# Kernel optimization log

Hardware: AMD Instinct MI355X
Metric: run time of the kernel (lower is better)

Reference implementation:

```python
import jax, jax.numpy as jnp
import numpy as np

B, S, D, F, E, CAP = 4, 2048, 1024, 4096, 8, 320


def setup_inputs() -> dict:
    key = jax.random.key(0)
    k1, k2, k3, k4 = jax.random.split(key, 4)
    return {
        "hidden_states": jax.random.normal(k1, (B, S, D), dtype=jnp.float32),
        "router_w": jax.random.normal(k2, (D, E), dtype=jnp.float32) * 0.02,
        "wi": jax.random.normal(k3, (E, D, F), dtype=jnp.float32) * 0.02,
        "wo": jax.random.normal(k4, (E, F, D), dtype=jnp.float32) * 0.02,
    }


def reference(hidden_states, router_w, wi, wo):
    # ---- Router (Switch top-1 with per-sequence expert capacity) ----
    b, s, d = hidden_states.shape
    e = router_w.shape[1]
    logits = hidden_states.astype(jnp.float32) @ router_w          # [B,S,E]
    probs = jax.nn.softmax(logits, axis=-1)                        # [B,S,E]
    expert_idx = jnp.argmax(probs, axis=-1)                        # [B,S]
    onehot = jax.nn.one_hot(expert_idx, e, dtype=jnp.int32)        # [B,S,E]
    priority = jnp.cumsum(onehot, axis=1)                          # cumsum over seq dim (dim=-2)
    keep = onehot * (priority <= CAP).astype(jnp.int32)            # capacity-masked router_mask

    # slot of each token within its chosen expert (0-based)
    slot = jnp.take_along_axis(priority, expert_idx[..., None], axis=-1)[..., 0] - 1  # [B,S]
    valid = slot < CAP                                             # dropped tokens exceed capacity
    slot_sc = jnp.where(valid, slot, CAP)                          # out-of-range -> dropped by scatter

    b_ar = jnp.broadcast_to(jnp.arange(b)[:, None], (b, s))
    s_ar = jnp.broadcast_to(jnp.arange(s)[None, :], (b, s))
    dispatch = jnp.zeros((b, e, CAP), jnp.int32).at[b_ar, expert_idx, slot_sc].set(
        s_ar.astype(jnp.int32), mode="drop")                       # [B,E,CAP] token index per slot
    slot_used = jnp.zeros((b, e, CAP), bool).at[b_ar, expert_idx, slot_sc].set(
        valid, mode="drop")                                        # [B,E,CAP]

    # ---- Dispatch: gather tokens into [B,E,CAP,D] ----
    xg = jax.vmap(lambda xb, ib: xb[ib])(hidden_states, dispatch)  # [B,E,CAP,D]

    # ---- Per-expert dense FFN (grouped GEMM) ----
    hg = jax.nn.relu(jnp.einsum("becd,edf->becf", xg, wi))         # [B,E,CAP,F]
    yg = jnp.einsum("becf,efd->becd", hg, wo)                      # [B,E,CAP,D]

    # ---- Combine: scatter expert outputs back; unrouted tokens keep input ----
    idx_back = jnp.where(slot_used, dispatch, s)                   # out-of-range -> dropped
    next_states = jax.vmap(
        lambda xb, ib, yb: xb.at[ib.reshape(-1)].set(yb.reshape(-1, d), mode="drop")
    )(hidden_states, idx_back, yg)                                 # [B,S,D]

    max_prob = jnp.max(probs, axis=-1, keepdims=True)              # [B,S,1]
    out = max_prob * next_states
    expert_index_out = jnp.argmax(keep, axis=-1)                   # [B,S] (0 for dropped tokens)
    return out, logits, expert_index_out
```

## Files before the change

### kernel.cpp

```cpp
#include <hip/hip_runtime.h>
#include <hip/hip_bf16.h>
#include <stdint.h>

#define B_ 4
#define S_ 2048
#define D_ 1024
#define F_ 4096
#define E_ 8
#define CAP_ 320
#define BS_ (B_*S_)
#define MPE 1280

typedef unsigned short u16;
typedef __attribute__((ext_vector_type(8))) short bf16x8;
typedef __attribute__((ext_vector_type(4))) float f32x4;
typedef __attribute__((ext_vector_type(4))) unsigned short u16x4;
typedef __attribute__((ext_vector_type(8))) unsigned short u16x8;

__device__ __forceinline__ u16 f2bf(float f) {
  union { float f; uint32_t u; } v; v.f = f;
  uint32_t r = (v.u + 0x7FFFu + ((v.u >> 16) & 1u)) >> 16;
  return (u16)r;
}

__device__ __forceinline__ void gload16(const void* g, void* l) {
  __builtin_amdgcn_global_load_lds(
      (const __attribute__((address_space(1))) uint32_t*)g,
      (__attribute__((address_space(3))) uint32_t*)l, 16, 0, 0);
}

__device__ __forceinline__ void transpose_block(
    const float* __restrict__ W, u16* __restrict__ WT,
    const int K, const int N, const int bid, void* ldsraw)
{
  float (*tile)[65] = (float(*)[65])ldsraw;
  const int tk = K >> 7, tn = N >> 6;
  const int e = bid / (tk * tn), r = bid % (tk * tn);
  const int k0 = (r / tn) << 7, n0 = (r % tn) << 6;
  const float* We = W + (size_t)e * K * N;
  u16* WTe = WT + (size_t)e * N * K;
  const int t = threadIdx.x;
  const int fr = t >> 2, c0 = (t & 3) * 16;
#pragma unroll
  for (int j = 0; j < 4; ++j) {
    const float4 v = *(const float4*)(We + (size_t)(k0 + fr) * N + n0 + c0 + j * 4);
    tile[fr][c0 + j*4 + 0] = v.x; tile[fr][c0 + j*4 + 1] = v.y;
    tile[fr][c0 + j*4 + 2] = v.z; tile[fr][c0 + j*4 + 3] = v.w;
  }
  __syncthreads();
  const int nr = t >> 3, kk0 = (t & 7) * 16;
  u16x8 o0, o1;
#pragma unroll
  for (int j = 0; j < 8; ++j) o0[j] = f2bf(tile[kk0 + j][nr]);
#pragma unroll
  for (int j = 0; j < 8; ++j) o1[j] = f2bf(tile[kk0 + 8 + j][nr]);
  u16* dst = WTe + (size_t)(n0 + nr) * K + k0 + kk0;
  *(u16x8*)dst = o0;
  *(u16x8*)(dst + 8) = o1;
}

__global__ __launch_bounds__(512) void transpose_kernel(
    const float* __restrict__ W, u16* __restrict__ WT, const int K, const int N)
{
  __shared__ __align__(16) float tile[128][65];
  transpose_block(W, WT, K, N, blockIdx.x, (void*)tile);
}

__global__ __launch_bounds__(512) void prep_kernel(
    const float* __restrict__ hs, const float* __restrict__ rw,
    const float* __restrict__ wi, u16* __restrict__ wT,
    float* __restrict__ logits, float* __restrict__ maxp,
    int* __restrict__ eidx, const int twiT)
{
  __shared__ __align__(16) float tile[128][65];
  if ((int)blockIdx.x < twiT) {
    transpose_block(wi, wT, D_, F_, blockIdx.x, (void*)tile);
    return;
  }
  const int wv = threadIdx.x >> 6, l = threadIdx.x & 63;
  const int token = (blockIdx.x - twiT) * 8 + wv;
  const float* row = hs + (size_t)token * D_;
  const float4* rw4 = (const float4*)rw;

  double acc0=0, acc1=0, acc2=0, acc3=0, acc4=0, acc5=0, acc6=0, acc7=0;
#pragma unroll
  for (int j = 0; j < 4; ++j) {
    const int d4 = l + j * 64;
    const float4 v = ((const float4*)row)[d4];
#pragma unroll
    for (int c = 0; c < 4; ++c) {
      const int d = d4 * 4 + c;
      const float x = (&v.x)[c];
      const float4 w0 = rw4[d * 2];
      const float4 w1 = rw4[d * 2 + 1];
      acc0 += (double)x * (double)w0.x;
      acc1 += (double)x * (double)w0.y;
      acc2 += (double)x * (double)w0.z;
      acc3 += (double)x * (double)w0.w;
      acc4 += (double)x * (double)w1.x;
      acc5 += (double)x * (double)w1.y;
      acc6 += (double)x * (double)w1.z;
      acc7 += (double)x * (double)w1.w;
    }
  }
  double acc[E_] = {acc0, acc1, acc2, acc3, acc4, acc5, acc6, acc7};
#pragma unroll
  for (int e = 0; e < E_; ++e) {
#pragma unroll
    for (int off = 32; off; off >>= 1)
      acc[e] += __shfl_xor(acc[e], off);
  }
  if (l == 0) {
    float lg[E_];
#pragma unroll
    for (int e = 0; e < E_; ++e) lg[e] = (float)acc[e];
    float lmax = lg[0]; int am = 0;
#pragma unroll
    for (int e = 1; e < E_; ++e) { if (lg[e] > lmax) { lmax = lg[e]; am = e; } }
    float sum = 0.f;
#pragma unroll
    for (int e = 0; e < E_; ++e) sum += expf(lg[e] - lmax);
#pragma unroll
    for (int e = 0; e < E_; ++e) logits[(size_t)token * E_ + e] = lg[e];
    maxp[token] = 1.0f / sum;
    eidx[token] = am;
  }
}

__global__ __launch_bounds__(256) void scan_kernel(
    const int* __restrict__ eidx, int* __restrict__ tok,
    float* __restrict__ eout, const float* __restrict__ hs,
    const float* __restrict__ maxp, float* __restrict__ out)
{
  const int b = blockIdx.x >> 3, e = blockIdx.x & 7;
  __shared__ int wsum[4];
  const int tid = threadIdx.x, wv = tid >> 6, l = tid & 63;
  for (int i = tid; i < CAP_; i += 256) tok[(b * E_ + e) * CAP_ + i] = -1;
  __syncthreads();
  int base = 0;
  for (int ch = 0; ch < S_ / 256; ++ch) {
    const int s = ch * 256 + tid;
    const bool p = (eidx[b * S_ + s] == e);
    const unsigned long long m = __ballot(p);
    const int lp = __popcll(m & ((1ULL << l) - 1ULL));
    if (l == 0) wsum[wv] = __popcll(m);
    __syncthreads();
    int pre = 0, tot = 0;
#pragma unroll
    for (int w = 0; w < 4; ++w) { if (w < wv) pre += wsum[w]; tot += wsum[w]; }
    if (p) {
      const int rank = base + pre + lp;
      if (rank < CAP_) {
        tok[(b * E_ + e) * CAP_ + rank] = s;
        eout[b * S_ + s] = (float)e;
      } else {
        eout[b * S_ + s] = 0.0f;
        const float mp = maxp[b * S_ + s];
        const float4* src = (const float4*)(hs + (size_t)(b * S_ + s) * D_);
        float4* dst = (float4*)(out + (size_t)(b * S_ + s) * D_);
        for (int j = 0; j < D_ / 4; ++j) {
          const float4 vv = src[j];
          float4 o; o.x = vv.x * mp; o.y = vv.y * mp; o.z = vv.z * mp; o.w = vv.w * mp;
          dst[j] = o;
        }
      }
    }
    base += tot;
    __syncthreads();
  }
}

__global__ __launch_bounds__(256) void gather_kernel(
    const float* __restrict__ hs, const int* __restrict__ tok,
    u16* __restrict__ Xg)
{
  const int bx = blockIdx.x;
  const int e = bx / MPE, r = bx % MPE;
  const int b = r / CAP_, c = r % CAP_;
  const int t = tok[(b * E_ + e) * CAP_ + c];
  const int d = threadIdx.x * 4;
  u16x4 o;
  if (t >= 0) {
    const float4 vv = *(const float4*)(hs + ((size_t)(b * S_ + t)) * D_ + d);
    o[0] = f2bf(vv.x); o[1] = f2bf(vv.y); o[2] = f2bf(vv.z); o[3] = f2bf(vv.w);
  } else {
    o[0] = 0; o[1] = 0; o[2] = 0; o[3] = 0;
  }
  *(u16x4*)(Xg + (size_t)bx * D_ + d) = o;
}

template<int MODE>
__global__ __launch_bounds__(512, 2) void moe_gemm8(
    const u16* __restrict__ Aall, const u16* __restrict__ Btall,
    u16* __restrict__ hgout, float* __restrict__ out,
    const int* __restrict__ tok, const float* __restrict__ maxp,
    const int K, const int ntn, const int gemm_blocks,
    const float* __restrict__ Wtr, u16* __restrict__ WTtr,
    const int tK, const int tN)
{
  __shared__ __align__(16) u16 lds[2][2][2][8192];

  if ((int)blockIdx.x >= gemm_blocks) {
    transpose_block(Wtr, WTtr, tK, tN, blockIdx.x - gemm_blocks, (void*)lds);
    return;
  }

  const int cpx = gemm_blocks >> 3;
  const int bid = blockIdx.x;
  const int swzb = (bid & 7) * cpx + (bid >> 3);
  const int bpe = 5 * ntn;
  const int e = swzb / bpe, rem = swzb % bpe;
  const int m0 = (rem / ntn) * 256, n0 = (rem % ntn) * 256;
  const int N = ntn * 256;

  const u16* Ae = Aall + (size_t)e * MPE * K;
  const u16* Be = Btall + (size_t)e * N * K;

  const int tid = threadIdx.x;
  const int wv = tid >> 6, l = tid & 63;
  const int wr = wv >> 2, wc = wv & 3;
  const int lr = l & 15, lk = l >> 4;
  const int rswz = ((lr >> 3) & 1) << 4;
  const int gs0 = tid ^ (((tid >> 5) & 1) << 1);
  const size_t goff = (size_t)((gs0 >> 2) & 127) * K + (size_t)((gs0 & 3) * 8);
  const int dwoff = wv * 512;

  const u16* pA0 = Ae + (size_t)m0 * K;
  const u16* pA1 = Ae + (size_t)(m0 + 128) * K;
  const u16* pB0 = Be + (size_t)n0 * K;
  const u16* pB1 = Be + (size_t)(n0 + 128) * K;

  const int NT = K >> 6;

  f32x4 acc[8][4];
#pragma unroll
  for (int i = 0; i < 8; ++i)
#pragma unroll
    for (int j = 0; j < 4; ++j) acc[i][j] = (f32x4){0.f, 0.f, 0.f, 0.f};

  bf16x8 fa[8], fb0[4], fb1[4];

#define LDSH(p, ab, h) (&lds[p][ab][h][0])

#define STAGE(dhalf, rb, tt) do {                                          \
    const u16* s_ = (rb) + goff + (size_t)((tt) * 64);                     \
    gload16(s_,      (dhalf) + dwoff);                                     \
    gload16(s_ + 32, (dhalf) + 4096 + dwoff);                              \
  } while (0)

#define READ_A(msub, p) do {                                               \
    _Pragma("unroll")                                                      \
    for (int mf = 0; mf < 4; ++mf)                                         \
      _Pragma("unroll")                                                    \
      for (int kk = 0; kk < 2; ++kk)                                       \
        fa[mf*2+kk] = *(const bf16x8*)&lds[p][0][wr]                       \
            [(kk*128 + (msub)*64 + mf*16 + lr)*32 + ((lk*8) ^ rswz)];      \
  } while (0)

#define READ_B(nsub, p, fb) do {                                           \
    _Pragma("unroll")                                                      \
    for (int nf = 0; nf < 2; ++nf)                                         \
      _Pragma("unroll")                                                    \
      for (int kk = 0; kk < 2; ++kk)                                       \
        fb[nf*2+kk] = *(const bf16x8*)&lds[p][1][wc>>1]                    \
            [(kk*128 + (wc&1)*64 + (nsub)*32 + nf*16 + lr)*32              \
             + ((lk*8) ^ rswz)];                                           \
  } while (0)

#define MFMA_Q(msub, nsub, fb) do {                                        \
    __builtin_amdgcn_s_setprio(1);                                         \
    _Pragma("unroll")                                                      \
    for (int mf = 0; mf < 4; ++mf)                                         \
      _Pragma("unroll")                                                    \
      for (int nf = 0; nf < 2; ++nf)                                       \
        _Pragma("unroll")                                                  \
        for (int kk = 0; kk < 2; ++kk)                                     \
          acc[(msub)*4+mf][(nsub)*2+nf] =                                  \
              __builtin_amdgcn_mfma_f32_16x16x32_bf16(                     \
                  fa[mf*2+kk], fb[nf*2+kk],                                \
                  acc[(msub)*4+mf][(nsub)*2+nf], 0, 0, 0);                 \
    __builtin_amdgcn_s_setprio(0);                                         \
  } while (0)

#define BAR() __builtin_amdgcn_s_barrier()
#define LGKM0() do { asm volatile("s_waitcnt lgkmcnt(0)" ::: "memory");    \
                     __builtin_amdgcn_sched_barrier(0); } while (0)
#define LGKM4() do { asm volatile("s_waitcnt lgkmcnt(4)" ::: "memory");    \
                     __builtin_amdgcn_sched_barrier(0); } while (0)
#define VM6() asm volatile("s_waitcnt vmcnt(6)" ::: "memory")
#define VM0() asm volatile("s_waitcnt vmcnt(0)" ::: "memory")

#define DO_TILE(p, pn, tc) do {                                            \
                                                                  \
    READ_A(0, p); READ_B(0, p, fb0); READ_B(1, p, fb1);                    \
    if ((tc) + 1 < NT) STAGE(LDSH(pn, 0, 1), pA1, (tc) + 1);               \
    BAR();                                                                 \
    LGKM4();                                                               \
    MFMA_Q(0, 0, fb0);                                                     \
    LGKM0();                                                               \
    MFMA_Q(0, 1, fb1);                                                     \
    BAR();                                                                 \
                                                                  \
    READ_A(1, p);                                                          \
    if ((tc) + 2 < NT) {                                                   \
      STAGE(LDSH(p, 1, 0), pB0, (tc) + 2);                                 \
      STAGE(LDSH(p, 1, 1), pB1, (tc) + 2);                                 \
      STAGE(LDSH(p, 0, 0), pA0, (tc) + 2);                                 \
    }                                                                      \
    BAR();                                                                 \
    LGKM0();                                                               \
    MFMA_Q(1, 0, fb0);                                                     \
    MFMA_Q(1, 1, fb1);                                                     \
    if ((tc) >= NT - 2) VM0(); else VM6();                                 \
    BAR();                                                                 \
  } while (0)

  STAGE(LDSH(0, 0, 0), pA0, 0);
  STAGE(LDSH(0, 0, 1), pA1, 0);
  STAGE(LDSH(0, 1, 0), pB0, 0);
  STAGE(LDSH(0, 1, 1), pB1, 0);
  STAGE(LDSH(1, 1, 0), pB0, 1);
  STAGE(LDSH(1, 1, 1), pB1, 1);
  STAGE(LDSH(1, 0, 0), pA0, 1);
  VM6(); BAR();

  for (int t = 0; t < NT; t += 2) {
    DO_TILE(0, 1, t);
    DO_TILE(1, 0, t + 1);
  }

  if (MODE == 1) {
#pragma unroll
    for (int i = 0; i < 8; ++i) {
#pragma unroll
      for (int r = 0; r < 4; ++r) {
        const int grow = m0 + wr * 128 + i * 16 + lk * 4 + r;
        u16* hrow = hgout + ((size_t)e * MPE + grow) * (size_t)N + n0 + wc * 64;
#pragma unroll
        for (int j = 0; j < 4; ++j)
          hrow[j * 16 + lr] = f2bf(fmaxf(acc[i][j][r], 0.0f));
      }
    }
  } else {
#pragma unroll
    for (int i = 0; i < 8; ++i) {
#pragma unroll
      for (int r = 0; r < 4; ++r) {
        const int grow = m0 + wr * 128 + i * 16 + lk * 4 + r;
        const int b = grow / CAP_, c = grow % CAP_;
        const int t = tok[(b * E_ + e) * CAP_ + c];
        if (t >= 0) {
          const float sc = maxp[b * S_ + t];
          float* orow = out + ((size_t)(b * S_ + t)) * D_ + n0 + wc * 64;
#pragma unroll
          for (int j = 0; j < 4; ++j)
            orow[j * 16 + lr] = sc * acc[i][j][r];
        }
      }
    }
  }
#undef LDSH
#undef STAGE
#undef READ_A
#undef READ_B
#undef MFMA_Q
#undef BAR
#undef LGKM0
#undef LGKM4
#undef VM6
#undef VM0
#undef DO_TILE
}

extern "C" void kernel_launch(void* const* d_in, const int* in_sizes, int n_in,
                              void* d_out, int out_size, void* d_ws, size_t ws_size,
                              hipStream_t stream)
{
  const float* hs = (const float*)d_in[0];
  const float* rw = (const float*)d_in[1];
  const float* wi = (const float*)d_in[2];
  const float* wo = (const float*)d_in[3];

  float* out    = (float*)d_out;
  float* logits = out + (size_t)BS_ * D_;
  float* eout   = logits + (size_t)BS_ * E_;

  uint8_t* ws = (uint8_t*)d_ws;
  int*   tok  = (int*)(ws + 0);
  float* maxp = (float*)(ws + 40960);
  int*   eidx = (int*)(ws + 73728);
  u16*   Xg   = (u16*)(ws + 131072);
  u16*   hg   = (u16*)(ws + 21102592);
  u16*   wiT  = (u16*)(ws + 104988672);
  if (ws_size < 172097536ULL) return;
  const bool big = ws_size >= 239206400ULL;
  u16* woT = big ? (u16*)(ws + 172097536) : wiT;

  const int twiT = E_ * (D_ / 128) * (F_ / 64);
  const int twoT = E_ * (F_ / 128) * (D_ / 64);
  const int g1 = E_ * 5 * (F_ / 256);
  const int g2 = E_ * 5 * (D_ / 256);

  prep_kernel<<<twiT + BS_ / 8, 512, 0, stream>>>(
      hs, rw, wi, wiT, logits, maxp, eidx, twiT);
  scan_kernel<<<B_ * E_, 256, 0, stream>>>(eidx, tok, eout, hs, maxp, out);
  gather_kernel<<<E_ * MPE, 256, 0, stream>>>(hs, tok, Xg);

  if (big) {
    moe_gemm8<1><<<g1 + twoT, 512, 0, stream>>>(
        Xg, wiT, hg, nullptr, tok, maxp, D_, F_ / 256, g1, wo, woT, F_, D_);
  } else {
    moe_gemm8<1><<<g1, 512, 0, stream>>>(
        Xg, wiT, hg, nullptr, tok, maxp, D_, F_ / 256, g1,
        nullptr, nullptr, 0, 0);
    transpose_kernel<<<twoT, 512, 0, stream>>>(wo, woT, F_, D_);
  }
  moe_gemm8<2><<<g2, 512, 0, stream>>>(
      hg, woT, nullptr, out, tok, maxp, F_, D_ / 256, g2,
      nullptr, nullptr, 0, 0);
}
```

Measured before the change: 354.7 us.

## Shrink GEMM tiles to 128x128 with 256-thread blocks and new pipeline

Replaces the 256x256-tile, 512-thread grouped GEMM with a 128x128-tile, 4-wave kernel. It uses a new interleaved LDS read / MFMA / prefetch schedule with quarter-wise A fragment loads and double-buffered staging. The transpose and prep kernels also move to 256-thread blocks, with each thread handling twice the elements. The aim is more blocks for better CU fill on the small expert GEMMs (1280 rows per expert), at the cost of lower per-block data reuse and more global traffic.

```diff
diff --git a/kernel.cpp b/kernel.cpp
--- a/kernel.cpp
+++ b/kernel.cpp
@@ -29,7 +29,7 @@
       (__attribute__((address_space(3))) uint32_t*)l, 16, 0, 0);
 }
 
-__device__ __forceinline__ void transpose_block(
+__device__ __forceinline__ void transpose_block256(
     const float* __restrict__ W, u16* __restrict__ WT,
     const int K, const int N, const int bid, void* ldsraw)
 {
@@ -40,33 +40,33 @@
   const float* We = W + (size_t)e * K * N;
   u16* WTe = WT + (size_t)e * N * K;
   const int t = threadIdx.x;
-  const int fr = t >> 2, c0 = (t & 3) * 16;
-#pragma unroll
-  for (int j = 0; j < 4; ++j) {
+  const int fr = t >> 1, c0 = (t & 1) * 32;
+#pragma unroll
+  for (int j = 0; j < 8; ++j) {
     const float4 v = *(const float4*)(We + (size_t)(k0 + fr) * N + n0 + c0 + j * 4);
     tile[fr][c0 + j*4 + 0] = v.x; tile[fr][c0 + j*4 + 1] = v.y;
     tile[fr][c0 + j*4 + 2] = v.z; tile[fr][c0 + j*4 + 3] = v.w;
   }
   __syncthreads();
-  const int nr = t >> 3, kk0 = (t & 7) * 16;
-  u16x8 o0, o1;
-#pragma unroll
-  for (int j = 0; j < 8; ++j) o0[j] = f2bf(tile[kk0 + j][nr]);
-#pragma unroll
-  for (int j = 0; j < 8; ++j) o1[j] = f2bf(tile[kk0 + 8 + j][nr]);
+  const int nr = t >> 2, kk0 = (t & 3) * 32;
   u16* dst = WTe + (size_t)(n0 + nr) * K + k0 + kk0;
-  *(u16x8*)dst = o0;
-  *(u16x8*)(dst + 8) = o1;
-}
-
-__global__ __launch_bounds__(512) void transpose_kernel(
+#pragma unroll
+  for (int h = 0; h < 4; ++h) {
+    u16x8 o;
+#pragma unroll
+    for (int j = 0; j < 8; ++j) o[j] = f2bf(tile[kk0 + h*8 + j][nr]);
+    *(u16x8*)(dst + h * 8) = o;
+  }
+}
+
+__global__ __launch_bounds__(256) void transpose_kernel(
     const float* __restrict__ W, u16* __restrict__ WT, const int K, const int N)
 {
   __shared__ __align__(16) float tile[128][65];
-  transpose_block(W, WT, K, N, blockIdx.x, (void*)tile);
-}
-
-__global__ __launch_bounds__(512) void prep_kernel(
+  transpose_block256(W, WT, K, N, blockIdx.x, (void*)tile);
+}
+
+__global__ __launch_bounds__(256) void prep_kernel(
     const float* __restrict__ hs, const float* __restrict__ rw,
     const float* __restrict__ wi, u16* __restrict__ wT,
     float* __restrict__ logits, float* __restrict__ maxp,
@@ -74,11 +74,11 @@
 {
   __shared__ __align__(16) float tile[128][65];
   if ((int)blockIdx.x < twiT) {
-    transpose_block(wi, wT, D_, F_, blockIdx.x, (void*)tile);
+    transpose_block256(wi, wT, D_, F_, blockIdx.x, (void*)tile);
     return;
   }
   const int wv = threadIdx.x >> 6, l = threadIdx.x & 63;
-  const int token = (blockIdx.x - twiT) * 8 + wv;
+  const int token = (blockIdx.x - twiT) * 4 + wv;
   const float* row = hs + (size_t)token * D_;
   const float4* rw4 = (const float4*)rw;
 
@@ -190,151 +190,126 @@
 }
 
 template<int MODE>
-__global__ __launch_bounds__(512, 2) void moe_gemm8(
+__global__ __launch_bounds__(256, 2) void moe_g(
     const u16* __restrict__ Aall, const u16* __restrict__ Btall,
     u16* __restrict__ hgout, float* __restrict__ out,
     const int* __restrict__ tok, const float* __restrict__ maxp,
     const int K, const int ntn, const int gemm_blocks,
-    const float* __restrict__ Wtr, u16* __restrict__ WTtr,
-    const int tK, const int tN)
-{
-  __shared__ __align__(16) u16 lds[2][2][2][8192];
+    const float* __restrict__ Wtr, u16* __restrict__ WTtr)
+{
+  __shared__ __align__(16) u16 lds[2][2][8192];
 
   if ((int)blockIdx.x >= gemm_blocks) {
-    transpose_block(Wtr, WTtr, tK, tN, blockIdx.x - gemm_blocks, (void*)lds);
+    transpose_block256(Wtr, WTtr, F_, D_, blockIdx.x - gemm_blocks, (void*)lds);
     return;
   }
 
+  const int NT = K >> 6;
   const int cpx = gemm_blocks >> 3;
   const int bid = blockIdx.x;
   const int swzb = (bid & 7) * cpx + (bid >> 3);
-  const int bpe = 5 * ntn;
+  const int bpe = 10 * ntn;
   const int e = swzb / bpe, rem = swzb % bpe;
-  const int m0 = (rem / ntn) * 256, n0 = (rem % ntn) * 256;
-  const int N = ntn * 256;
+  const int m0 = (rem / ntn) * 128, n0 = (rem % ntn) * 128;
+  const int N = ntn * 128;
 
   const u16* Ae = Aall + (size_t)e * MPE * K;
   const u16* Be = Btall + (size_t)e * N * K;
 
   const int tid = threadIdx.x;
   const int wv = tid >> 6, l = tid & 63;
-  const int wr = wv >> 2, wc = wv & 3;
+  const int wr = wv >> 1, wc = wv & 1;
   const int lr = l & 15, lk = l >> 4;
   const int rswz = ((lr >> 3) & 1) << 4;
   const int gs0 = tid ^ (((tid >> 5) & 1) << 1);
-  const size_t goff = (size_t)((gs0 >> 2) & 127) * K + (size_t)((gs0 & 3) * 8);
+  const size_t goff = (size_t)((gs0 >> 2) & 63) * K + (size_t)((gs0 & 3) * 8);
   const int dwoff = wv * 512;
 
-  const u16* pA0 = Ae + (size_t)m0 * K;
-  const u16* pA1 = Ae + (size_t)(m0 + 128) * K;
-  const u16* pB0 = Be + (size_t)n0 * K;
-  const u16* pB1 = Be + (size_t)(n0 + 128) * K;
-
-  const int NT = K >> 6;
-
-  f32x4 acc[8][4];
-#pragma unroll
-  for (int i = 0; i < 8; ++i)
+  const u16* pA = Ae + (size_t)m0 * K;
+  const u16* pB = Be + (size_t)n0 * K;
+  const size_t r64 = (size_t)64 * K;
+
+  f32x4 acc[4][4];
+#pragma unroll
+  for (int i = 0; i < 4; ++i)
 #pragma unroll
     for (int j = 0; j < 4; ++j) acc[i][j] = (f32x4){0.f, 0.f, 0.f, 0.f};
 
-  bf16x8 fa[8], fb0[4], fb1[4];
-
-#define LDSH(p, ab, h) (&lds[p][ab][h][0])
-
-#define STAGE(dhalf, rb, tt) do {                                          \
+  bf16x8 faA[2], faB[2], fb[8];
+
+#define BAR() __builtin_amdgcn_s_barrier()
+#define LGKMN(n) do { asm volatile("s_waitcnt lgkmcnt(" #n ")" ::: "memory"); \
+                      __builtin_amdgcn_sched_barrier(0); } while (0)
+#define VMW(n) asm volatile("s_waitcnt vmcnt(" #n ")" ::: "memory")
+
+#define STAGE_T(dst, rb, tt) do {                                          \
     const u16* s_ = (rb) + goff + (size_t)((tt) * 64);                     \
-    gload16(s_,      (dhalf) + dwoff);                                     \
-    gload16(s_ + 32, (dhalf) + 4096 + dwoff);                              \
-  } while (0)
-
-#define READ_A(msub, p) do {                                               \
+    gload16(s_,             (dst) + dwoff);             \
+    gload16(s_ + r64,       (dst) + 2048 + dwoff);     \
+    gload16(s_ + 32,        (dst) + 4096 + dwoff);      \
+    gload16(s_ + r64 + 32,  (dst) + 6144 + dwoff);     \
+  } while (0)
+
+#define READ_AQ(q, p, fa_) do {                                            \
     _Pragma("unroll")                                                      \
-    for (int mf = 0; mf < 4; ++mf)                                         \
+    for (int kk = 0; kk < 2; ++kk)                                         \
+      fa_[kk] = *(const bf16x8*)&lds[p][0]                                 \
+          [(kk*128 + wr*64 + (q)*16 + lr)*32 + ((lk*8) ^ rswz)];           \
+  } while (0)
+
+#define READ_B_ALL(p) do {                                                 \
+    _Pragma("unroll")                                                      \
+    for (int nf = 0; nf < 4; ++nf)                                         \
       _Pragma("unroll")                                                    \
       for (int kk = 0; kk < 2; ++kk)                                       \
-        fa[mf*2+kk] = *(const bf16x8*)&lds[p][0][wr]                       \
-            [(kk*128 + (msub)*64 + mf*16 + lr)*32 + ((lk*8) ^ rswz)];      \
-  } while (0)
-
-#define READ_B(nsub, p, fb) do {                                           \
+        fb[nf*2+kk] = *(const bf16x8*)&lds[p][1]                           \
+            [(kk*128 + wc*64 + nf*16 + lr)*32 + ((lk*8) ^ rswz)];          \
+  } while (0)
+
+#define MFMA_P(q, fa_) do {                                                \
+    __builtin_amdgcn_s_setprio(1);                                         \
     _Pragma("unroll")                                                      \
-    for (int nf = 0; nf < 2; ++nf)                                         \
+    for (int nf = 0; nf < 4; ++nf)                                         \
       _Pragma("unroll")                                                    \
       for (int kk = 0; kk < 2; ++kk)                                       \
-        fb[nf*2+kk] = *(const bf16x8*)&lds[p][1][wc>>1]                    \
-            [(kk*128 + (wc&1)*64 + (nsub)*32 + nf*16 + lr)*32              \
-             + ((lk*8) ^ rswz)];                                           \
-  } while (0)
-
-#define MFMA_Q(msub, nsub, fb) do {                                        \
-    __builtin_amdgcn_s_setprio(1);                                         \
-    _Pragma("unroll")                                                      \
-    for (int mf = 0; mf < 4; ++mf)                                         \
-      _Pragma("unroll")                                                    \
-      for (int nf = 0; nf < 2; ++nf)                                       \
-        _Pragma("unroll")                                                  \
-        for (int kk = 0; kk < 2; ++kk)                                     \
-          acc[(msub)*4+mf][(nsub)*2+nf] =                                  \
-              __builtin_amdgcn_mfma_f32_16x16x32_bf16(                     \
-                  fa[mf*2+kk], fb[nf*2+kk],                                \
-                  acc[(msub)*4+mf][(nsub)*2+nf], 0, 0, 0);                 \
+        acc[q][nf] = __builtin_amdgcn_mfma_f32_16x16x32_bf16(              \
+            fa_[kk], fb[nf*2+kk], acc[q][nf], 0, 0, 0);                    \
     __builtin_amdgcn_s_setprio(0);                                         \
   } while (0)
 
-#define BAR() __builtin_amdgcn_s_barrier()
-#define LGKM0() do { asm volatile("s_waitcnt lgkmcnt(0)" ::: "memory");    \
-                     __builtin_amdgcn_sched_barrier(0); } while (0)
-#define LGKM4() do { asm volatile("s_waitcnt lgkmcnt(4)" ::: "memory");    \
-                     __builtin_amdgcn_sched_barrier(0); } while (0)
-#define VM6() asm volatile("s_waitcnt vmcnt(6)" ::: "memory")
-#define VM0() asm volatile("s_waitcnt vmcnt(0)" ::: "memory")
-
-#define DO_TILE(p, pn, tc) do {                                            \
-                                                                  \
-    READ_A(0, p); READ_B(0, p, fb0); READ_B(1, p, fb1);                    \
-    if ((tc) + 1 < NT) STAGE(LDSH(pn, 0, 1), pA1, (tc) + 1);               \
+#define DO_T(p, pn, tc) do {                                               \
+    READ_AQ(1, p, faB);                                                    \
+    if ((tc) + 1 < NT) STAGE_T(&lds[pn][0][0], pA, (tc) + 1);              \
+    LGKMN(2); MFMA_P(0, faA);                                              \
+    READ_AQ(2, p, faA);                                                    \
+    LGKMN(2); MFMA_P(1, faB);                                              \
     BAR();                                                                 \
-    LGKM4();                                                               \
-    MFMA_Q(0, 0, fb0);                                                     \
-    LGKM0();                                                               \
-    MFMA_Q(0, 1, fb1);                                                     \
+    READ_AQ(3, p, faB);                                                    \
+    if ((tc) + 2 < NT) STAGE_T(&lds[p][1][0], pB, (tc) + 2);               \
+    LGKMN(2); MFMA_P(2, faA);                                              \
+    LGKMN(0); MFMA_P(3, faB);                                              \
+    if ((tc) >= NT - 2) VMW(0); else VMW(4);                               \
     BAR();                                                                 \
-                                                                  \
-    READ_A(1, p);                                                          \
-    if ((tc) + 2 < NT) {                                                   \
-      STAGE(LDSH(p, 1, 0), pB0, (tc) + 2);                                 \
-      STAGE(LDSH(p, 1, 1), pB1, (tc) + 2);                                 \
-      STAGE(LDSH(p, 0, 0), pA0, (tc) + 2);                                 \
-    }                                                                      \
-    BAR();                                                                 \
-    LGKM0();                                                               \
-    MFMA_Q(1, 0, fb0);                                                     \
-    MFMA_Q(1, 1, fb1);                                                     \
-    if ((tc) >= NT - 2) VM0(); else VM6();                                 \
-    BAR();                                                                 \
-  } while (0)
-
-  STAGE(LDSH(0, 0, 0), pA0, 0);
-  STAGE(LDSH(0, 0, 1), pA1, 0);
-  STAGE(LDSH(0, 1, 0), pB0, 0);
-  STAGE(LDSH(0, 1, 1), pB1, 0);
-  STAGE(LDSH(1, 1, 0), pB0, 1);
-  STAGE(LDSH(1, 1, 1), pB1, 1);
-  STAGE(LDSH(1, 0, 0), pA0, 1);
-  VM6(); BAR();
+    if ((tc) + 1 < NT) { READ_B_ALL(pn); READ_AQ(0, pn, faA); }            \
+  } while (0)
+
+  STAGE_T(&lds[0][0][0], pA, 0);
+  STAGE_T(&lds[0][1][0], pB, 0);
+  STAGE_T(&lds[1][1][0], pB, 1);
+  VMW(4); BAR();
+  READ_B_ALL(0); READ_AQ(0, 0, faA);
 
   for (int t = 0; t < NT; t += 2) {
-    DO_TILE(0, 1, t);
-    DO_TILE(1, 0, t + 1);
+    DO_T(0, 1, t);
+    DO_T(1, 0, t + 1);
   }
 
   if (MODE == 1) {
 #pragma unroll
-    for (int i = 0; i < 8; ++i) {
+    for (int i = 0; i < 4; ++i) {
 #pragma unroll
       for (int r = 0; r < 4; ++r) {
-        const int grow = m0 + wr * 128 + i * 16 + lk * 4 + r;
+        const int grow = m0 + wr * 64 + i * 16 + lk * 4 + r;
         u16* hrow = hgout + ((size_t)e * MPE + grow) * (size_t)N + n0 + wc * 64;
 #pragma unroll
         for (int j = 0; j < 4; ++j)
@@ -343,10 +318,10 @@
     }
   } else {
 #pragma unroll
-    for (int i = 0; i < 8; ++i) {
+    for (int i = 0; i < 4; ++i) {
 #pragma unroll
       for (int r = 0; r < 4; ++r) {
-        const int grow = m0 + wr * 128 + i * 16 + lk * 4 + r;
+        const int grow = m0 + wr * 64 + i * 16 + lk * 4 + r;
         const int b = grow / CAP_, c = grow % CAP_;
         const int t = tok[(b * E_ + e) * CAP_ + c];
         if (t >= 0) {
@@ -359,17 +334,14 @@
       }
     }
   }
-#undef LDSH
-#undef STAGE
-#undef READ_A
-#undef READ_B
-#undef MFMA_Q
 #undef BAR
-#undef LGKM0
-#undef LGKM4
-#undef VM6
-#undef VM0
-#undef DO_TILE
+#undef LGKMN
+#undef VMW
+#undef STAGE_T
+#undef READ_AQ
+#undef READ_B_ALL
+#undef MFMA_P
+#undef DO_T
 }
 
 extern "C" void kernel_launch(void* const* d_in, const int* in_sizes, int n_in,
@@ -398,24 +370,22 @@
 
   const int twiT = E_ * (D_ / 128) * (F_ / 64);
   const int twoT = E_ * (F_ / 128) * (D_ / 64);
-  const int g1 = E_ * 5 * (F_ / 256);
-  const int g2 = E_ * 5 * (D_ / 256);
-
-  prep_kernel<<<twiT + BS_ / 8, 512, 0, stream>>>(
+  const int g1 = E_ * (MPE / 128) * (F_ / 128);
+  const int g2 = E_ * (MPE / 128) * (D_ / 128);
+
+  prep_kernel<<<twiT + BS_ / 4, 256, 0, stream>>>(
       hs, rw, wi, wiT, logits, maxp, eidx, twiT);
   scan_kernel<<<B_ * E_, 256, 0, stream>>>(eidx, tok, eout, hs, maxp, out);
   gather_kernel<<<E_ * MPE, 256, 0, stream>>>(hs, tok, Xg);
 
   if (big) {
-    moe_gemm8<1><<<g1 + twoT, 512, 0, stream>>>(
-        Xg, wiT, hg, nullptr, tok, maxp, D_, F_ / 256, g1, wo, woT, F_, D_);
+    moe_g<1><<<g1 + twoT, 256, 0, stream>>>(
+        Xg, wiT, hg, nullptr, tok, maxp, D_, F_ / 128, g1, wo, woT);
   } else {
-    moe_gemm8<1><<<g1, 512, 0, stream>>>(
-        Xg, wiT, hg, nullptr, tok, maxp, D_, F_ / 256, g1,
-        nullptr, nullptr, 0, 0);
-    transpose_kernel<<<twoT, 512, 0, stream>>>(wo, woT, F_, D_);
-  }
-  moe_gemm8<2><<<g2, 512, 0, stream>>>(
-      hg, woT, nullptr, out, tok, maxp, F_, D_ / 256, g2,
-      nullptr, nullptr, 0, 0);
-}
+    moe_g<1><<<g1, 256, 0, stream>>>(
+        Xg, wiT, hg, nullptr, tok, maxp, D_, F_ / 128, g1, nullptr, nullptr);
+    transpose_kernel<<<twoT, 256, 0, stream>>>(wo, woT, F_, D_);
+  }
+  moe_g<2><<<g2, 256, 0, stream>>>(
+      hg, woT, nullptr, out, tok, maxp, F_, D_ / 128, g2, nullptr, nullptr);
+}
```

New measurement: 386.3 us. 1.09x slower.
